# Performance work log

Hardware: AMD Instinct MI355X
Metric: run time of the kernel (lower is better)

The kernel has to match this reference:

```python
import jax, jax.numpy as jnp
import numpy as np

SOS = 1  # vocab.word2idx[SYM_SOS]


def _lstm_cell(x, h, c, Wih, Whh, b):
    # PyTorch LSTMCell gate order: i, f, g, o
    g = x @ Wih.T + h @ Whh.T + b
    i, f, gg, o = jnp.split(g, 4, axis=-1)
    c2 = jax.nn.sigmoid(f) * c + jax.nn.sigmoid(i) * jnp.tanh(gg)
    h2 = jax.nn.sigmoid(o) * jnp.tanh(c2)
    return h2, c2


def _attention(q, m, Wq, Wm, b, v):
    # additive attention: q [B,Dq], m [B,N,Dm] -> context [B,Dm]
    e = jnp.tanh((q @ Wq)[:, None, :] + m @ Wm + b)      # [B,N,H]
    score = jnp.einsum('bnh,h->bn', e, v)                # [B,N]
    a = jax.nn.softmax(score, axis=-1)
    return jnp.einsum('bn,bnd->bd', a, m)


def setup_inputs() -> dict:
    key = jax.random.key(0)
    ks = iter(jax.random.split(key, 32))
    B, T, V = 128, 20, 20000
    DI, DW, H = 512, 512, 1024
    s = 0.02
    d = {}
    d['img_feats'] = jax.random.normal(next(ks), (B, 36, DI), jnp.float32)
    d['ppl_feats'] = jax.random.normal(next(ks), (B, 100, DI), jnp.float32)
    d['answer_hint'] = jax.random.normal(next(ks), (B, DW), jnp.float32)
    d['question'] = jax.random.randint(next(ks), (B, T), 0, V)
    d['emb'] = jax.random.normal(next(ks), (V, DW), jnp.float32) * s
    d['pool_Wq'] = jax.random.normal(next(ks), (DW, DW), jnp.float32) * s
    d['pool_Wm'] = jax.random.normal(next(ks), (DI, DW), jnp.float32) * s
    d['pool_b'] = jnp.zeros((DW,), jnp.float32)
    d['pool_v'] = jax.random.normal(next(ks), (DW,), jnp.float32) * s
    d['img_Wq'] = jax.random.normal(next(ks), (H, H), jnp.float32) * s
    d['img_Wm'] = jax.random.normal(next(ks), (DI, H), jnp.float32) * s
    d['img_b'] = jnp.zeros((H,), jnp.float32)
    d['img_v'] = jax.random.normal(next(ks), (H,), jnp.float32) * s
    d['ppl_Wq'] = jax.random.normal(next(ks), (H, H), jnp.float32) * s
    d['ppl_Wm'] = jax.random.normal(next(ks), (DI, H), jnp.float32) * s
    d['ppl_b'] = jnp.zeros((H,), jnp.float32)
    d['ppl_v'] = jax.random.normal(next(ks), (H,), jnp.float32) * s
    d['vis_Wih'] = jax.random.normal(next(ks), (4 * H, DI + DW), jnp.float32) * s
    d['vis_Whh'] = jax.random.normal(next(ks), (4 * H, H), jnp.float32) * s
    d['vis_b'] = jnp.zeros((4 * H,), jnp.float32)
    d['lang_Wih'] = jax.random.normal(next(ks), (4 * H, H + DI), jnp.float32) * s
    d['lang_Whh'] = jax.random.normal(next(ks), (4 * H, H), jnp.float32) * s
    d['lang_b'] = jnp.zeros((4 * H,), jnp.float32)
    d['proj_W'] = jax.random.normal(next(ks), (H, V), jnp.float32) * s
    d['proj_b'] = jnp.zeros((V,), jnp.float32)
    return d


def reference(img_feats, ppl_feats, answer_hint, question, emb,
              pool_Wq, pool_Wm, pool_b, pool_v,
              img_Wq, img_Wm, img_b, img_v,
              ppl_Wq, ppl_Wm, ppl_b, ppl_v,
              vis_Wih, vis_Whh, vis_b,
              lang_Wih, lang_Whh, lang_b,
              proj_W, proj_b):
    B, T = question.shape
    H = vis_Whh.shape[1]
    # pooled image feature from answer hint (computed once)
    img_pool = _attention(answer_hint, img_feats, pool_Wq, pool_Wm, pool_b, pool_v)
    # teacher forcing inputs: SOS then question[:, :-1]
    tokens_in = jnp.concatenate(
        [jnp.full((B, 1), SOS, question.dtype), question[:, :-1]], axis=1)

    def step(carry, tok):
        h_vis, c_vis, h_lang, c_lang = carry
        dec_emb = jax.nn.relu(emb[tok])                          # [B,DW]
        x_vis = jnp.concatenate([img_pool, dec_emb], axis=-1)
        h_vis, c_vis = _lstm_cell(x_vis, h_vis, c_vis, vis_Wih, vis_Whh, vis_b)
        image_attn = _attention(h_vis, img_feats, img_Wq, img_Wm, img_b, img_v)
        ppl_attn = _attention(h_vis, ppl_feats, ppl_Wq, ppl_Wm, ppl_b, ppl_v)
        x_lang = jnp.concatenate([image_attn + ppl_attn, h_vis], axis=-1)
        h_lang, c_lang = _lstm_cell(x_lang, h_lang, c_lang, lang_Wih, lang_Whh, lang_b)
        logp = jax.nn.log_softmax(h_lang @ proj_W + proj_b, axis=-1)
        return (h_vis, c_vis, h_lang, c_lang), (logp, jnp.argmax(logp, axis=-1))

    z = jnp.zeros((B, H), img_feats.dtype)
    _, (logps, toks) = jax.lax.scan(step, (z, z, z, z), tokens_in.T)
    return jnp.transpose(logps, (1, 0, 2)), toks.T


if __name__ == '__main__':
    out = reference(**setup_inputs())
    print(out[0].shape, out[1].shape)
```

## Files before the change

### kernel.cpp

```cpp
#include <hip/hip_runtime.h>
#include <cstddef>
#include <cstdint>

using u16 = unsigned short;
typedef float    f32x4 __attribute__((ext_vector_type(4)));
typedef _Float16 f16x8 __attribute__((ext_vector_type(8)));
typedef u16      us8   __attribute__((ext_vector_type(8)));

constexpr int B  = 128;
constexpr int T  = 20;
constexpr int V  = 20000;
constexpr int DW = 512;
constexpr int H  = 1024;
constexpr int G4 = 4096;
constexpr int NI = 36;
constexpr int NP = 100;
constexpr int SOS = 1;

__device__ __forceinline__ float sigf(float x) { return 1.0f / (1.0f + expf(-x)); }
__device__ __forceinline__ u16 f16bits(_Float16 h) { u16 u; __builtin_memcpy(&u, &h, 2); return u; }
__device__ __forceinline__ float h2f(u16 u) { _Float16 h; __builtin_memcpy(&h, &u, 2); return (float)h; }

template<bool WSIDE>
__device__ __forceinline__ void split1(float x, u16& b0, u16& b1, u16& b2) {
    _Float16 h  = (_Float16)x;
    float    hf = (float)h;
    _Float16 lo = (_Float16)((x - hf) * 64.0f);
    _Float16 hs = (_Float16)(hf * (1.0f / 64.0f));
    b0 = f16bits(h);
    if constexpr (WSIDE) { b1 = f16bits(hs); b2 = f16bits(lo); }
    else                 { b1 = f16bits(lo); b2 = f16bits(hs); }
}

template<int BM, int BN, bool HAS_ADD, bool HAS_BIAS, int NSW = 0, bool OUTF16 = false>
__global__ __launch_bounds__(256)
void gemm3(const u16* __restrict__ A, const u16* __restrict__ Bt,
           const float* __restrict__ Add, const float* __restrict__ bias,
           void* __restrict__ Cv, int N, int K3)
{
    __shared__ __align__(16) u16 As[BM * 64];
    __shared__ __align__(16) u16 Bs[BN * 64];
    constexpr int FR = BM / 32, FC = BN / 32, PA = BM / 32, PB = BN / 32;
    const int tid  = threadIdx.x;
    int bx = blockIdx.x, by = blockIdx.y;
    if constexpr (NSW > 0) {
        const int nt = (int)gridDim.x, mt = (int)gridDim.y;
        const int lin = by * nt + bx;
        const int sc0 = (lin / (NSW * mt)) * NSW;
        const int w   = (NSW < nt - sc0) ? NSW : (nt - sc0);
        const int r   = lin - sc0 * mt;
        bx = sc0 + r % w;
        by = r / w;
    }
    const int bm   = by * BM, bn = bx * BN;
    const int lane = tid & 63, wid = tid >> 6;
    const int wm   = (wid >> 1) * (BM / 2), wn = (wid & 1) * (BN / 2);
    const int srow = tid >> 3;
    const int scol = (tid & 7) * 8;

    f32x4 acc[FR][FC] = {};
    us8 ra[PA], rb[PB];

    auto ldg = [&](int k0) {
#pragma unroll
        for (int p = 0; p < PA; ++p)
            ra[p] = *(const us8*)(A + (size_t)(bm + p * 32 + srow) * K3 + k0 + scol);
#pragma unroll
        for (int p = 0; p < PB; ++p) {
            int n = bn + p * 32 + srow; if (n > N - 1) n = N - 1;
            rb[p] = *(const us8*)(Bt + (size_t)n * K3 + k0 + scol);
        }
    };
    ldg(0);

    for (int k0 = 0; k0 < K3; k0 += 64) {
        __syncthreads();
#pragma unroll
        for (int p = 0; p < PA; ++p) {
            const int row = p * 32 + srow;
            *(us8*)((char*)As + row * 128 + ((scol * 2) ^ ((row & 7) << 4))) = ra[p];
        }
#pragma unroll
        for (int p = 0; p < PB; ++p) {
            const int row = p * 32 + srow;
            *(us8*)((char*)Bs + row * 128 + ((scol * 2) ^ ((row & 7) << 4))) = rb[p];
        }
        __syncthreads();
        if (k0 + 64 < K3) ldg(k0 + 64);
#pragma unroll
        for (int ks = 0; ks < 2; ++ks) {
            f16x8 af[FR], bf[FC];
#pragma unroll
            for (int m = 0; m < FR; ++m) {
                const int row = wm + m * 16 + (lane & 15);
                const int cb  = (ks * 64 + ((lane >> 4) << 4)) ^ ((row & 7) << 4);
                af[m] = *(const f16x8*)((const char*)As + row * 128 + cb);
            }
#pragma unroll
            for (int n = 0; n < FC; ++n) {
                const int row = wn + n * 16 + (lane & 15);
                const int cb  = (ks * 64 + ((lane >> 4) << 4)) ^ ((row & 7) << 4);
                bf[n] = *(const f16x8*)((const char*)Bs + row * 128 + cb);
            }
#pragma unroll
            for (int m = 0; m < FR; ++m)
#pragma unroll
                for (int n = 0; n < FC; ++n)
                    acc[m][n] = __builtin_amdgcn_mfma_f32_16x16x32_f16(af[m], bf[n], acc[m][n], 0, 0, 0);
        }
    }
#pragma unroll
    for (int m = 0; m < FR; ++m) {
        const int r0 = bm + wm + m * 16 + ((lane >> 4) << 2);
#pragma unroll
        for (int n = 0; n < FC; ++n) {
            const int c = bn + wn + n * 16 + (lane & 15);
            if (c < N) {
#pragma unroll
                for (int j = 0; j < 4; ++j) {
                    float v = acc[m][n][j];
                    if constexpr (HAS_ADD)  v += Add[(size_t)(r0 + j) * N + c];
                    if constexpr (HAS_BIAS) v += bias[c];
                    if constexpr (OUTF16)
                        ((u16*)Cv)[(size_t)(r0 + j) * N + c] = f16bits((_Float16)v);
                    else
                        ((float*)Cv)[(size_t)(r0 + j) * N + c] = v;
                }
            }
        }
    }
}

template<int EPI, int BN, int BK>
__device__ __forceinline__ void gemm_core(
    u16* __restrict__ As, u16* __restrict__ Bs,
    const u16* __restrict__ A, const u16* __restrict__ Bt,
    const float* __restrict__ Add, const float* __restrict__ bias,
    float* __restrict__ CS, u16* __restrict__ o1, u16* __restrict__ o2,
    int N, int K3, int t, int bx, int by)
{
    constexpr int NA8  = BK / 32;
    constexpr int TPRB = 256 / BN;
    constexpr int NB8  = (BK / TPRB) / 8;
    constexpr int NFC  = BN / 16;
    const int tid  = threadIdx.x;
    const int bn   = bx * BN, bm = by * 64;
    const int lane = tid & 63, wv = tid >> 6;
    const int rowA = tid >> 2;
    const int scA  = (tid & 3) * (BK / 4);
    const int rowB = tid / TPRB;
    const int scB  = (tid % TPRB) * (BK / TPRB);
    const int swzA = (rowA & 7) << 4;
    const int swzB = (rowB & 7) << 4;
    const u16* Ap = A  + (size_t)(bm + rowA) * K3 + scA;
    const u16* Bp = Bt + (size_t)(bn + rowB) * K3 + scB;
    char* Awp = (char*)As + rowA * (BK * 2);
    char* Bwp = (char*)Bs + rowB * (BK * 2);
    const int arow = wv * 16 + (lane & 15);
    const char* Arp = (const char*)As + arow * (BK * 2);
    const int aswz = (arow & 7) << 4;
    const int jl   = lane & 15;

    f32x4 acc[NFC] = {};
    us8 ra[NA8], rb[NB8];
#pragma unroll
    for (int i = 0; i < NA8; ++i) ra[i] = *(const us8*)(Ap + 8 * i);
#pragma unroll
    for (int i = 0; i < NB8; ++i) rb[i] = *(const us8*)(Bp + 8 * i);

    for (int k0 = 0; k0 < K3; k0 += BK) {
        __syncthreads();
#pragma unroll
        for (int i = 0; i < NA8; ++i)
            *(us8*)(Awp + ((scA * 2 + 16 * i) ^ swzA)) = ra[i];
#pragma unroll
        for (int i = 0; i < NB8; ++i)
            *(us8*)(Bwp + ((scB * 2 + 16 * i) ^ swzB)) = rb[i];
        __syncthreads();
        if (k0 + BK < K3) {
#pragma unroll
            for (int i = 0; i < NA8; ++i) ra[i] = *(const us8*)(Ap + k0 + BK + 8 * i);
#pragma unroll
            for (int i = 0; i < NB8; ++i) rb[i] = *(const us8*)(Bp + k0 + BK + 8 * i);
        }
#pragma unroll
        for (int ks = 0; ks < BK / 32; ++ks) {
            const int cb = ks * 64 + ((lane >> 4) << 4);
            const f16x8 af = *(const f16x8*)(Arp + (cb ^ aswz));
#pragma unroll
            for (int g = 0; g < NFC; ++g) {
                const int brow = g * 16 + jl;
                const f16x8 bf = *(const f16x8*)((const char*)Bs + brow * (BK * 2) + (cb ^ ((brow & 7) << 4)));
                acc[g] = __builtin_amdgcn_mfma_f32_16x16x32_f16(af, bf, acc[g], 0, 0, 0);
            }
        }
    }
    const int rb0 = bm + wv * 16 + ((lane >> 4) << 2);
    if constexpr (EPI == 0) {
#pragma unroll
        for (int g = 0; g < NFC; ++g) {
            const int c = bn + g * 16 + jl;
#pragma unroll
            for (int jj = 0; jj < 4; ++jj)
                CS[(size_t)(rb0 + jj) * N + c] = acc[g][jj];
        }
    } else {
        const int j = bx * 16 + jl;
#pragma unroll
        for (int jj = 0; jj < 4; ++jj) {
            const int b = rb0 + jj;
            float gi = acc[0][jj], gf = acc[1][jj], gg = acc[2][jj], go = acc[3][jj];
            if constexpr (EPI == 1) {
                const float* ap = Add + (size_t)b * 4096 + bn + jl;
                gi += ap[0]; gf += ap[16]; gg += ap[32]; go += ap[48];
            } else {
                const float* bp = bias + bn + jl;
                gi += bp[0]; gf += bp[16]; gg += bp[32]; go += bp[48];
            }
            const float c = sigf(gf) * CS[b * 1024 + j] + sigf(gi) * tanhf(gg);
            const float h = sigf(go) * tanhf(c);
            CS[b * 1024 + j] = c;
            u16 b0, b1, b2; split1<false>(h, b0, b1, b2);
            if constexpr (EPI == 1) {
                u16* a = o1 + (size_t)b * 3072 + j;
                a[0] = b0; a[1024] = b1; a[2048] = b2;
                u16* x = o2 + (size_t)b * 7680 + 512 + j;
                x[0] = b0; x[2560] = b1; x[5120] = b2;
            } else {
                u16* x = o1 + (size_t)b * 7680 + 1536 + j;
                x[0] = b0; x[2560] = b1; x[5120] = b2;
                u16* hh = o2 + ((size_t)b * T + t) * 3072 + j;
                hh[0] = b0; hh[1024] = b1; hh[2048] = b2;
            }
        }
    }
}

__global__ __launch_bounds__(256)
void gemm_q(const u16* __restrict__ A, const u16* __restrict__ Bt,
            float* __restrict__ CS, int N, int K3)
{
    __shared__ __align__(16) u16 As[64 * 384];
    __shared__ __align__(16) u16 Bs[32 * 384];
    gemm_core<0, 32, 384>(As, Bs, A, Bt, nullptr, nullptr, CS, nullptr, nullptr,
                          N, K3, 0, blockIdx.x, blockIdx.y);
}

__global__ __launch_bounds__(256)
void step_combo(const u16* __restrict__ lang_A, const u16* __restrict__ langW3,
                const float* __restrict__ lang_bi, float* __restrict__ c_lang,
                u16* __restrict__ lang_o1, u16* __restrict__ h3_all,
                const u16* __restrict__ vis_A, const u16* __restrict__ visWhh3,
                const float* __restrict__ g_pre_t, float* __restrict__ c_vis,
                u16* __restrict__ vis_o1, u16* __restrict__ vis_o2, int t)
{
    __shared__ __align__(16) u16 As[64 * 384];
    __shared__ __align__(16) u16 Bs[64 * 384];
    if (blockIdx.z == 0) {
        if (t >= 1)
            gemm_core<2, 64, 384>(As, Bs, lang_A, langW3, nullptr, lang_bi,
                                  c_lang, lang_o1, h3_all, G4, 7680, t - 1,
                                  blockIdx.x, blockIdx.y);
    } else {
        if (t < T)
            gemm_core<1, 64, 384>(As, Bs, vis_A, visWhh3, g_pre_t, nullptr,
                                  c_vis, vis_o1, vis_o2, G4, 3072, t,
                                  blockIdx.x, blockIdx.y);
    }
}

template<bool WSIDE>
__global__ __launch_bounds__(256)
void split3_rows(const float* __restrict__ src, int ld, int K8,
                 u16* __restrict__ out, int Kt, int coloff)
{
    const int idx = blockIdx.x * 256 + threadIdx.x;
    const int r = idx / K8, kk = (idx - r * K8) * 8;
    const float* s = src + (size_t)r * ld + kk;
    const float4 x0 = *(const float4*)s, x1 = *(const float4*)(s + 4);
    float xs[8] = {x0.x, x0.y, x0.z, x0.w, x1.x, x1.y, x1.z, x1.w};
    us8 h, m, l;
#pragma unroll
    for (int j = 0; j < 8; ++j) { u16 a, b, c; split1<WSIDE>(xs[j], a, b, c); h[j]=a; m[j]=b; l[j]=c; }
    u16* o = out + (size_t)r * (3 * Kt) + coloff + kk;
    *(us8*)o = h; *(us8*)(o + Kt) = m; *(us8*)(o + 2 * Kt) = l;
}

__global__ __launch_bounds__(256)
void split3_lstm(const float* __restrict__ src, int ld, int K8,
                 u16* __restrict__ out, int Kt, int coloff)
{
    const int idx = blockIdx.x * 256 + threadIdx.x;
    const int r = idx / K8, kk = (idx - r * K8) * 8;
    const int g = r >> 10, j = r & 1023;
    const int orow = ((j >> 4) << 6) + (g << 4) + (j & 15);
    const float* s = src + (size_t)r * ld + kk;
    const float4 x0 = *(const float4*)s, x1 = *(const float4*)(s + 4);
    float xs[8] = {x0.x, x0.y, x0.z, x0.w, x1.x, x1.y, x1.z, x1.w};
    us8 h, m, l;
#pragma unroll
    for (int jj = 0; jj < 8; ++jj) { u16 a, b, c; split1<true>(xs[jj], a, b, c); h[jj]=a; m[jj]=b; l[jj]=c; }
    u16* o = out + (size_t)orow * (3 * Kt) + coloff + kk;
    *(us8*)o = h; *(us8*)(o + Kt) = m; *(us8*)(o + 2 * Kt) = l;
}

__global__ __launch_bounds__(256)
void permute_bias_lstm(const float* __restrict__ b, float* __restrict__ out)
{
    const int c = blockIdx.x * 256 + threadIdx.x;
    const int jg = c >> 6, g = (c >> 4) & 3, jlo = c & 15;
    out[c] = b[g * 1024 + jg * 16 + jlo];
}

__global__ __launch_bounds__(256)
void transpose_split3_w(const float* __restrict__ W, int N, int K,
                        u16* __restrict__ out)
{
    const int n0 = blockIdx.x * 64, k0 = blockIdx.y * 64;
    const int tid = threadIdx.x;
    __shared__ float ts[64][65];
    for (int i = 0; i < 16; ++i) {
        const int idx = i * 256 + tid;
        const int kl = idx >> 6, nl = idx & 63;
        float v = 0.f;
        if (n0 + nl < N) v = W[(size_t)(k0 + kl) * N + n0 + nl];
        ts[nl][kl] = v;
    }
    __syncthreads();
    for (int i = 0; i < 2; ++i) {
        const int idx = i * 256 + tid;
        const int nl = idx >> 3, kc = (idx & 7) * 8;
        if (n0 + nl < N) {
            us8 h, m, l;
#pragma unroll
            for (int j = 0; j < 8; ++j) {
                u16 a, b, c; split1<true>(ts[nl][kc + j], a, b, c);
                h[j] = a; m[j] = b; l[j] = c;
            }
            u16* o = out + (size_t)(n0 + nl) * (3 * K) + k0 + kc;
            *(us8*)o = h; *(us8*)(o + K) = m; *(us8*)(o + 2 * K) = l;
        }
    }
}

__global__ __launch_bounds__(256)
void embed_relu3(const int* __restrict__ question, const float* __restrict__ emb,
                 u16* __restrict__ demb3)
{
    const int idx = blockIdx.x * 256 + threadIdx.x;
    const int r = idx >> 6, kk = (idx & 63) * 8;
    const int t = r / B, b = r - t * B;
    const int tok = (t == 0) ? SOS : question[b * T + t - 1];
    const float* s = emb + (size_t)tok * DW + kk;
    const float4 x0 = *(const float4*)s, x1 = *(const float4*)(s + 4);
    float xs[8] = {x0.x, x0.y, x0.z, x0.w, x1.x, x1.y, x1.z, x1.w};
    us8 h, m, l;
#pragma unroll
    for (int j = 0; j < 8; ++j) {
        u16 a, b2, c; split1<false>(fmaxf(xs[j], 0.f), a, b2, c);
        h[j] = a; m[j] = b2; l[j] = c;
    }
    u16* o = demb3 + (size_t)r * 1536 + kk;
    *(us8*)o = h; *(us8*)(o + 512) = m; *(us8*)(o + 1024) = l;
}

__global__ __launch_bounds__(256)
void attn_score(const float* __restrict__ q, int qld,
                const float* __restrict__ mW, const float* __restrict__ v,
                float* __restrict__ score, int Nn, int Hd)
{
    const int n = blockIdx.x, b = blockIdx.y;
    const float* qp = q + (size_t)b * qld;
    const float* mp = mW + ((size_t)b * Nn + n) * Hd;
    float s = 0.f;
    for (int h = threadIdx.x; h < Hd; h += 256)
        s += tanhf(qp[h] + mp[h]) * v[h];
    __shared__ float red[4];
    const int lane = threadIdx.x & 63, wv = threadIdx.x >> 6;
    for (int o = 32; o; o >>= 1) s += __shfl_down(s, o, 64);
    if (lane == 0) red[wv] = s;
    __syncthreads();
    if (threadIdx.x == 0) score[(size_t)b * Nn + n] = red[0] + red[1] + red[2] + red[3];
}

__global__ __launch_bounds__(256)
void attn_ctx_pool(const float* __restrict__ score, const float* __restrict__ m,
                   u16* __restrict__ out3, int Nn)
{
    constexpr int D = 512;
    const int b = blockIdx.x;
    __shared__ float aw[128];
    __shared__ float red[8];
    const int tid = threadIdx.x, lane = tid & 63, wv = tid >> 6;
    float mx = -3.4e38f;
    for (int n = tid; n < Nn; n += 256) mx = fmaxf(mx, score[(size_t)b * Nn + n]);
    for (int o = 32; o; o >>= 1) mx = fmaxf(mx, __shfl_down(mx, o, 64));
    if (lane == 0) red[wv] = mx;
    __syncthreads();
    mx = fmaxf(fmaxf(red[0], red[1]), fmaxf(red[2], red[3]));
    float se = 0.f;
    for (int n = tid; n < Nn; n += 256) {
        float e = expf(score[(size_t)b * Nn + n] - mx);
        aw[n] = e; se += e;
    }
    for (int o = 32; o; o >>= 1) se += __shfl_down(se, o, 64);
    if (lane == 0) red[4 + wv] = se;
    __syncthreads();
    const float inv = 1.0f / (red[4] + red[5] + red[6] + red[7]);
    for (int d = tid; d < D; d += 256) {
        float s = 0.f;
        for (int n = 0; n < Nn; ++n) s += aw[n] * m[((size_t)b * Nn + n) * D + d];
        s *= inv;
        u16 b0, b1, b2; split1<false>(s, b0, b1, b2);
        u16* o = out3 + (size_t)b * 1536 + d;
        o[0] = b0; o[512] = b1; o[1024] = b2;
    }
}

__global__ __launch_bounds__(512)
void attn_fused(const float* __restrict__ qbuf,
                const u16* __restrict__ img_mW, const u16* __restrict__ ppl_mW,
                const float* __restrict__ img_v, const float* __restrict__ ppl_v,
                const float* __restrict__ img_feats, const float* __restrict__ ppl_feats,
                u16* __restrict__ x3)
{
    const int b = blockIdx.x;
    const int tid = threadIdx.x, lane = tid & 63, wv = tid >> 6;
    __shared__ float qs[2048];
    __shared__ float vs[2048];
    __shared__ float aw[136];
    __shared__ float awn[136];

    for (int i = tid; i < 2048; i += 512) {
        qs[i] = qbuf[(size_t)b * 2048 + i];
        vs[i] = (i < 1024) ? img_v[i] : ppl_v[i - 1024];
    }
    __syncthreads();

    for (int n = wv; n < NI; n += 8) {
        const u16* mp = img_mW + ((size_t)b * NI + n) * 1024;
        float s = 0.f;
#pragma unroll
        for (int u = 0; u < 2; ++u) {
            const int h = (lane + 64 * u) * 8;
            const us8 m8 = *(const us8*)(mp + h);
#pragma unroll
            for (int j = 0; j < 8; ++j)
                s += tanhf(qs[h + j] + h2f(m8[j])) * vs[h + j];
        }
        for (int o = 1; o < 64; o <<= 1) s += __shfl_xor(s, o, 64);
        if (lane == 0) aw[n] = s;
    }
    for (int n = wv; n < NP; n += 8) {
        const u16* mp = ppl_mW + ((size_t)b * NP + n) * 1024;
        float s = 0.f;
#pragma unroll
        for (int u = 0; u < 2; ++u) {
            const int h = (lane + 64 * u) * 8;
            const us8 m8 = *(const us8*)(mp + h);
#pragma unroll
            for (int j = 0; j < 8; ++j)
                s += tanhf(qs[1024 + h + j] + h2f(m8[j])) * vs[1024 + h + j];
        }
        for (int o = 1; o < 64; o <<= 1) s += __shfl_xor(s, o, 64);
        if (lane == 0) aw[36 + n] = s;
    }
    __syncthreads();

    if (wv == 0) {
        const float x = (lane < NI) ? aw[lane] : -3.4e38f;
        float mx = x;
        for (int o = 1; o < 64; o <<= 1) mx = fmaxf(mx, __shfl_xor(mx, o, 64));
        const float e = (lane < NI) ? expf(x - mx) : 0.f;
        float ss = e;
        for (int o = 1; o < 64; o <<= 1) ss += __shfl_xor(ss, o, 64);
        if (lane < NI) awn[lane] = e / ss;
    } else if (wv == 1) {
        const float x0 = aw[36 + lane];
        const float x1 = (lane < NP - 64) ? aw[100 + lane] : -3.4e38f;
        float mx = fmaxf(x0, x1);
        for (int o = 1; o < 64; o <<= 1) mx = fmaxf(mx, __shfl_xor(mx, o, 64));
        const float e0 = expf(x0 - mx);
        const float e1 = (lane < NP - 64) ? expf(x1 - mx) : 0.f;
        float ss = e0 + e1;
        for (int o = 1; o < 64; o <<= 1) ss += __shfl_xor(ss, o, 64);
        awn[36 + lane] = e0 / ss;
        if (lane < NP - 64) awn[100 + lane] = e1 / ss;
    }
    __syncthreads();

    {
        const int d = tid;
        float s = 0.f;
        const float* ip = img_feats + (size_t)b * NI * 512 + d;
#pragma unroll 4
        for (int n = 0; n < NI; ++n) s += awn[n] * ip[n * 512];
        const float* pp = ppl_feats + (size_t)b * NP * 512 + d;
#pragma unroll 4
        for (int n = 0; n < NP; ++n) s += awn[36 + n] * pp[n * 512];
        u16 b0, b1, b2; split1<false>(s, b0, b1, b2);
        u16* o = x3 + (size_t)b * 7680 + d;
        o[0] = b0; o[2560] = b1; o[5120] = b2;
    }
}

__global__ __launch_bounds__(256)
void add_bcast(float* __restrict__ g_pre, const float* __restrict__ g_const)
{
    const int idx = blockIdx.x * 256 + threadIdx.x;
    const int bg = idx % (B * G4 / 4);
    float4 a = ((float4*)g_pre)[idx];
    const float4 c = ((const float4*)g_const)[bg];
    a.x += c.x; a.y += c.y; a.z += c.z; a.w += c.w;
    ((float4*)g_pre)[idx] = a;
}

__global__ __launch_bounds__(256)
void zero_f(float* __restrict__ p) { p[blockIdx.x * 256 + threadIdx.x] = 0.f; }

__global__ __launch_bounds__(256)
void zero_u32(unsigned int* __restrict__ p) { p[blockIdx.x * 256 + threadIdx.x] = 0u; }

__global__ __launch_bounds__(256)
void logsm_argmax(float* __restrict__ out)
{
    const int r = blockIdx.x;
    float* row = out + (size_t)r * V;
    const int tid = threadIdx.x, lane = tid & 63, wv = tid >> 6;
    float m = -3.4e38f, s = 0.f; int mi = 0;
    for (int i4 = tid; i4 < V / 4; i4 += 256) {
        const float4 x4 = ((const float4*)row)[i4];
        const float xs[4] = {x4.x, x4.y, x4.z, x4.w};
#pragma unroll
        for (int j = 0; j < 4; ++j) {
            const float x = xs[j];
            if (x > m) { s = s * expf(m - x) + 1.f; m = x; mi = i4 * 4 + j; }
            else       s += expf(x - m);
        }
    }
    for (int o = 1; o < 64; o <<= 1) {
        const float m2 = __shfl_xor(m, o, 64);
        const float s2 = __shfl_xor(s, o, 64);
        const int  mi2 = __shfl_xor(mi, o, 64);
        if (m2 > m || (m2 == m && mi2 < mi)) { s = s2 + s * expf(m - m2); m = m2; mi = mi2; }
        else s += s2 * expf(m2 - m);
    }
    __shared__ float sm[4], ssm[4]; __shared__ int smi[4];
    __shared__ float lse_sh; __shared__ int mi_sh;
    if (lane == 0) { sm[wv] = m; ssm[wv] = s; smi[wv] = mi; }
    __syncthreads();
    if (tid == 0) {
        float M = sm[0], S = ssm[0]; int MI = smi[0];
        for (int w = 1; w < 4; ++w) {
            if (sm[w] > M || (sm[w] == M && smi[w] < MI)) { S = ssm[w] + S * expf(M - sm[w]); M = sm[w]; MI = smi[w]; }
            else S += ssm[w] * expf(sm[w] - M);
        }
        lse_sh = M + logf(S); mi_sh = MI;
    }
    __syncthreads();
    const float lse = lse_sh;
    for (int i4 = tid; i4 < V / 4; i4 += 256) {
        float4 x4 = ((const float4*)row)[i4];
        x4.x -= lse; x4.y -= lse; x4.z -= lse; x4.w -= lse;
        ((float4*)row)[i4] = x4;
    }
    if (tid == 0) out[(size_t)B * T * V + r] = (float)mi_sh;
}

extern "C" void kernel_launch(void* const* d_in, const int* in_sizes, int n_in,
                              void* d_out, int out_size, void* d_ws, size_t ws_size,
                              hipStream_t stream)
{
    (void)in_sizes; (void)n_in; (void)out_size; (void)ws_size;

    const float* img_feats   = (const float*)d_in[0];
    const float* ppl_feats   = (const float*)d_in[1];
    const float* answer_hint = (const float*)d_in[2];
    const int*   question    = (const int*)d_in[3];
    const float* emb         = (const float*)d_in[4];
    const float* pool_Wq     = (const float*)d_in[5];
    const float* pool_Wm     = (const float*)d_in[6];
    const float* pool_b      = (const float*)d_in[7];
    const float* pool_v      = (const float*)d_in[8];
    const float* img_Wq      = (const float*)d_in[9];
    const float* img_Wm      = (const float*)d_in[10];
    const float* img_b       = (const float*)d_in[11];
    const float* img_v       = (const float*)d_in[12];
    const float* ppl_Wq      = (const float*)d_in[13];
    const float* ppl_Wm      = (const float*)d_in[14];
    const float* ppl_b       = (const float*)d_in[15];
    const float* ppl_v       = (const float*)d_in[16];
    const float* vis_Wih     = (const float*)d_in[17];
    const float* vis_Whh     = (const float*)d_in[18];
    const float* vis_b       = (const float*)d_in[19];
    const float* lang_Wih    = (const float*)d_in[20];
    const float* lang_Whh    = (const float*)d_in[21];
    const float* lang_b      = (const float*)d_in[22];
    const float* proj_W      = (const float*)d_in[23];
    const float* proj_b      = (const float*)d_in[24];

    float* out = (float*)d_out;
    float* ws  = (float*)d_ws;

    size_t off = 0;
    auto alloc = [&](size_t nf) { size_t r = off; off += (nf + 63) & ~(size_t)63; return r; };
    const size_t regionX = off;
    float* g_pre   = ws + alloc((size_t)T * B * G4);
    float* pool_mW = ws + alloc((size_t)B * NI * DW);
    u16*   demb3   = (u16*)(ws + alloc((size_t)T * B * 1536 / 2));
    u16*   hint3   = (u16*)(ws + alloc((size_t)B * 1536 / 2));
    u16*   poolWq3t= (u16*)(ws + alloc((size_t)512 * 1536 / 2));
    u16*   poolWm3t= (u16*)(ws + alloc((size_t)512 * 1536 / 2));
    u16*   visdemb3= (u16*)(ws + alloc((size_t)G4 * 1536 / 2));
    u16*   vispool3= (u16*)(ws + alloc((size_t)G4 * 1536 / 2));
    u16* img_mW    = (u16*)(ws + alloc((size_t)B * NI * H / 2));
    u16* ppl_mW    = (u16*)(ws + alloc((size_t)B * NP * H / 2));
    u16* img3      = (u16*)(ws + alloc((size_t)B * NI * 1536 / 2));
    u16* ppl3      = (u16*)(ws + alloc((size_t)B * NP * 1536 / 2));
    u16* imgpool3  = (u16*)(ws + alloc((size_t)B * 1536 / 2));
    u16* visWhh3   = (u16*)(ws + alloc((size_t)G4 * 3072 / 2));
    u16* langW3    = (u16*)(ws + alloc((size_t)G4 * 7680 / 2));
    u16* wq3t      = (u16*)(ws + alloc((size_t)2048 * 3072 / 2));
    u16* imgWm3t   = (u16*)(ws + alloc((size_t)1024 * 1536 / 2));
    u16* pplWm3t   = (u16*)(ws + alloc((size_t)1024 * 1536 / 2));
    float* c_vis   = ws + alloc((size_t)B * H);
    float* c_lang  = ws + alloc((size_t)B * H);
    u16* a3        = (u16*)(ws + alloc((size_t)2 * B * 3072 / 2));
    u16* x3        = (u16*)(ws + alloc((size_t)2 * B * 7680 / 2));
    u16* h3_all    = (u16*)(ws + alloc((size_t)B * T * 3072 / 2));
    float* qbuf    = ws + alloc((size_t)B * 2048);
    float* g_const = ws + alloc((size_t)B * G4);
    float* vis_bi  = ws + alloc((size_t)G4);
    float* lang_bi = ws + alloc((size_t)G4);
    float* pool_qW = ws + alloc((size_t)B * DW);
    float* pool_sc = ws + alloc((size_t)B * NI);
    u16* projW3t   = (u16*)(ws + regionX);

    const dim3 blk(256);

    zero_f<<<dim3((2 * B * H) / 256), blk, 0, stream>>>(c_vis);
    zero_u32<<<dim3((2 * B * 3072 + 2 * B * 7680) / 2 / 256), blk, 0, stream>>>((unsigned int*)a3);

    embed_relu3<<<dim3(T * B * 64 / 256), blk, 0, stream>>>(question, emb, demb3);
    permute_bias_lstm<<<dim3(16), blk, 0, stream>>>(vis_b, vis_bi);
    permute_bias_lstm<<<dim3(16), blk, 0, stream>>>(lang_b, lang_bi);
    split3_lstm<<<dim3(G4 * 64 / 256), blk, 0, stream>>>(vis_Wih + 512, 1024, 64, visdemb3, 512, 0);
    split3_lstm<<<dim3(G4 * 64 / 256), blk, 0, stream>>>(vis_Wih, 1024, 64, vispool3, 512, 0);
    split3_lstm<<<dim3(G4 * 128 / 256), blk, 0, stream>>>(vis_Whh, 1024, 128, visWhh3, 1024, 0);
    split3_lstm<<<dim3(G4 * 192 / 256), blk, 0, stream>>>(lang_Wih, 1536, 192, langW3, 2560, 0);
    split3_lstm<<<dim3(G4 * 128 / 256), blk, 0, stream>>>(lang_Whh, 1024, 128, langW3, 2560, 1536);
    split3_rows<false><<<dim3(B * NI * 64 / 256), blk, 0, stream>>>(img_feats, 512, 64, img3, 512, 0);
    split3_rows<false><<<dim3(B * NP * 64 / 256), blk, 0, stream>>>(ppl_feats, 512, 64, ppl3, 512, 0);
    split3_rows<false><<<dim3(B * 64 / 256), blk, 0, stream>>>(answer_hint, 512, 64, hint3, 512, 0);
    transpose_split3_w<<<dim3(8, 8), blk, 0, stream>>>(pool_Wq, 512, 512, poolWq3t);
    transpose_split3_w<<<dim3(8, 8), blk, 0, stream>>>(pool_Wm, 512, 512, poolWm3t);
    transpose_split3_w<<<dim3(16, 8), blk, 0, stream>>>(img_Wm, 1024, 512, imgWm3t);
    transpose_split3_w<<<dim3(16, 8), blk, 0, stream>>>(ppl_Wm, 1024, 512, pplWm3t);
    transpose_split3_w<<<dim3(16, 16), blk, 0, stream>>>(img_Wq, 1024, 1024, wq3t);
    transpose_split3_w<<<dim3(16, 16), blk, 0, stream>>>(ppl_Wq, 1024, 1024, wq3t + (size_t)1024 * 3072);

    gemm3<128, 128, false, true><<<dim3(32, 20), blk, 0, stream>>>(demb3, visdemb3, nullptr, vis_bi, g_pre, G4, 1536);
    gemm3<64, 64, false, false><<<dim3(8, 2), blk, 0, stream>>>(hint3, poolWq3t, nullptr, nullptr, pool_qW, 512, 1536);
    gemm3<128, 128, false, true><<<dim3(4, 36), blk, 0, stream>>>(img3, poolWm3t, nullptr, pool_b, pool_mW, 512, 1536);
    attn_score<<<dim3(NI, B), blk, 0, stream>>>(pool_qW, 512, pool_mW, pool_v, pool_sc, NI, 512);
    attn_ctx_pool<<<dim3(B), blk, 0, stream>>>(pool_sc, img_feats, imgpool3, NI);
    gemm3<64, 64, false, false><<<dim3(64, 2), blk, 0, stream>>>(imgpool3, vispool3, nullptr, nullptr, g_const, G4, 1536);
    add_bcast<<<dim3(T * B * G4 / 4 / 256), blk, 0, stream>>>(g_pre, g_const);
    gemm3<128, 128, false, true, 0, true><<<dim3(8, 36), blk, 0, stream>>>(img3, imgWm3t, nullptr, img_b, img_mW, H, 1536);
    gemm3<128, 128, false, true, 0, true><<<dim3(8, 100), blk, 0, stream>>>(ppl3, pplWm3t, nullptr, ppl_b, ppl_mW, H, 1536);

    for (int t = 0; t <= T; ++t) {
        u16* lang_A  = x3 + (size_t)((t + 1) & 1) * B * 7680;
        u16* lang_o1 = x3 + (size_t)(t & 1) * B * 7680;
        u16* vis_A   = a3 + (size_t)(t & 1) * B * 3072;
        u16* vis_o1  = a3 + (size_t)((t + 1) & 1) * B * 3072;
        u16* vis_o2  = x3 + (size_t)(t & 1) * B * 7680;
        const float* gp = g_pre + (size_t)(t < T ? t : 0) * B * G4;
        step_combo<<<dim3(64, 2, 2), blk, 0, stream>>>(
            lang_A, langW3, lang_bi, c_lang, lang_o1, h3_all,
            vis_A, visWhh3, gp, c_vis, vis_o1, vis_o2, t);
        if (t < T) {
            gemm_q<<<dim3(64, 2), blk, 0, stream>>>(vis_o1, wq3t, qbuf, 2048, 3072);
            attn_fused<<<dim3(B), dim3(512), 0, stream>>>(qbuf, img_mW, ppl_mW, img_v, ppl_v,
                                                          img_feats, ppl_feats, vis_o2);
        }
    }

    transpose_split3_w<<<dim3(313, 16), blk, 0, stream>>>(proj_W, V, 1024, projW3t);
    gemm3<128, 128, false, true, 20><<<dim3(157, 20), blk, 0, stream>>>(
        h3_all, projW3t, nullptr, proj_b, out, V, 3072);
    logsm_argmax<<<dim3(B * T), blk, 0, stream>>>(out);
}
```

Measured before the change: 3.658 ms.

## Reschedule recurrent step into two fused kernels overlapping attention, vis and lang LSTM

```diff
diff --git a/kernel.cpp b/kernel.cpp
--- a/kernel.cpp
+++ b/kernel.cpp
@@ -133,10 +133,10 @@
 
 template<int EPI, int BN, int BK>
 __device__ __forceinline__ void gemm_core(
-    u16* __restrict__ As, u16* __restrict__ Bs,
-    const u16* __restrict__ A, const u16* __restrict__ Bt,
-    const float* __restrict__ Add, const float* __restrict__ bias,
-    float* __restrict__ CS, u16* __restrict__ o1, u16* __restrict__ o2,
+    u16* As, u16* Bs,
+    const u16* A, const u16* Bt,
+    const float* Add, const float* bias,
+    float* CS, u16* o1, u16* o2,
     int N, int K3, int t, int bx, int by)
 {
     constexpr int NA8  = BK / 32;
@@ -236,208 +236,26 @@
     }
 }
 
-__global__ __launch_bounds__(256)
-void gemm_q(const u16* __restrict__ A, const u16* __restrict__ Bt,
-            float* __restrict__ CS, int N, int K3)
-{
-    __shared__ __align__(16) u16 As[64 * 384];
-    __shared__ __align__(16) u16 Bs[32 * 384];
-    gemm_core<0, 32, 384>(As, Bs, A, Bt, nullptr, nullptr, CS, nullptr, nullptr,
-                          N, K3, 0, blockIdx.x, blockIdx.y);
-}
-
-__global__ __launch_bounds__(256)
-void step_combo(const u16* __restrict__ lang_A, const u16* __restrict__ langW3,
-                const float* __restrict__ lang_bi, float* __restrict__ c_lang,
-                u16* __restrict__ lang_o1, u16* __restrict__ h3_all,
-                const u16* __restrict__ vis_A, const u16* __restrict__ visWhh3,
-                const float* __restrict__ g_pre_t, float* __restrict__ c_vis,
-                u16* __restrict__ vis_o1, u16* __restrict__ vis_o2, int t)
-{
-    __shared__ __align__(16) u16 As[64 * 384];
-    __shared__ __align__(16) u16 Bs[64 * 384];
-    if (blockIdx.z == 0) {
-        if (t >= 1)
-            gemm_core<2, 64, 384>(As, Bs, lang_A, langW3, nullptr, lang_bi,
-                                  c_lang, lang_o1, h3_all, G4, 7680, t - 1,
-                                  blockIdx.x, blockIdx.y);
-    } else {
-        if (t < T)
-            gemm_core<1, 64, 384>(As, Bs, vis_A, visWhh3, g_pre_t, nullptr,
-                                  c_vis, vis_o1, vis_o2, G4, 3072, t,
-                                  blockIdx.x, blockIdx.y);
-    }
-}
-
-template<bool WSIDE>
-__global__ __launch_bounds__(256)
-void split3_rows(const float* __restrict__ src, int ld, int K8,
-                 u16* __restrict__ out, int Kt, int coloff)
-{
-    const int idx = blockIdx.x * 256 + threadIdx.x;
-    const int r = idx / K8, kk = (idx - r * K8) * 8;
-    const float* s = src + (size_t)r * ld + kk;
-    const float4 x0 = *(const float4*)s, x1 = *(const float4*)(s + 4);
-    float xs[8] = {x0.x, x0.y, x0.z, x0.w, x1.x, x1.y, x1.z, x1.w};
-    us8 h, m, l;
-#pragma unroll
-    for (int j = 0; j < 8; ++j) { u16 a, b, c; split1<WSIDE>(xs[j], a, b, c); h[j]=a; m[j]=b; l[j]=c; }
-    u16* o = out + (size_t)r * (3 * Kt) + coloff + kk;
-    *(us8*)o = h; *(us8*)(o + Kt) = m; *(us8*)(o + 2 * Kt) = l;
-}
-
-__global__ __launch_bounds__(256)
-void split3_lstm(const float* __restrict__ src, int ld, int K8,
-                 u16* __restrict__ out, int Kt, int coloff)
-{
-    const int idx = blockIdx.x * 256 + threadIdx.x;
-    const int r = idx / K8, kk = (idx - r * K8) * 8;
-    const int g = r >> 10, j = r & 1023;
-    const int orow = ((j >> 4) << 6) + (g << 4) + (j & 15);
-    const float* s = src + (size_t)r * ld + kk;
-    const float4 x0 = *(const float4*)s, x1 = *(const float4*)(s + 4);
-    float xs[8] = {x0.x, x0.y, x0.z, x0.w, x1.x, x1.y, x1.z, x1.w};
-    us8 h, m, l;
-#pragma unroll
-    for (int jj = 0; jj < 8; ++jj) { u16 a, b, c; split1<true>(xs[jj], a, b, c); h[jj]=a; m[jj]=b; l[jj]=c; }
-    u16* o = out + (size_t)orow * (3 * Kt) + coloff + kk;
-    *(us8*)o = h; *(us8*)(o + Kt) = m; *(us8*)(o + 2 * Kt) = l;
-}
-
-__global__ __launch_bounds__(256)
-void permute_bias_lstm(const float* __restrict__ b, float* __restrict__ out)
-{
-    const int c = blockIdx.x * 256 + threadIdx.x;
-    const int jg = c >> 6, g = (c >> 4) & 3, jlo = c & 15;
-    out[c] = b[g * 1024 + jg * 16 + jlo];
-}
-
-__global__ __launch_bounds__(256)
-void transpose_split3_w(const float* __restrict__ W, int N, int K,
-                        u16* __restrict__ out)
-{
-    const int n0 = blockIdx.x * 64, k0 = blockIdx.y * 64;
-    const int tid = threadIdx.x;
-    __shared__ float ts[64][65];
-    for (int i = 0; i < 16; ++i) {
-        const int idx = i * 256 + tid;
-        const int kl = idx >> 6, nl = idx & 63;
-        float v = 0.f;
-        if (n0 + nl < N) v = W[(size_t)(k0 + kl) * N + n0 + nl];
-        ts[nl][kl] = v;
-    }
-    __syncthreads();
-    for (int i = 0; i < 2; ++i) {
-        const int idx = i * 256 + tid;
-        const int nl = idx >> 3, kc = (idx & 7) * 8;
-        if (n0 + nl < N) {
-            us8 h, m, l;
-#pragma unroll
-            for (int j = 0; j < 8; ++j) {
-                u16 a, b, c; split1<true>(ts[nl][kc + j], a, b, c);
-                h[j] = a; m[j] = b; l[j] = c;
-            }
-            u16* o = out + (size_t)(n0 + nl) * (3 * K) + k0 + kc;
-            *(us8*)o = h; *(us8*)(o + K) = m; *(us8*)(o + 2 * K) = l;
-        }
-    }
-}
-
-__global__ __launch_bounds__(256)
-void embed_relu3(const int* __restrict__ question, const float* __restrict__ emb,
-                 u16* __restrict__ demb3)
-{
-    const int idx = blockIdx.x * 256 + threadIdx.x;
-    const int r = idx >> 6, kk = (idx & 63) * 8;
-    const int t = r / B, b = r - t * B;
-    const int tok = (t == 0) ? SOS : question[b * T + t - 1];
-    const float* s = emb + (size_t)tok * DW + kk;
-    const float4 x0 = *(const float4*)s, x1 = *(const float4*)(s + 4);
-    float xs[8] = {x0.x, x0.y, x0.z, x0.w, x1.x, x1.y, x1.z, x1.w};
-    us8 h, m, l;
-#pragma unroll
-    for (int j = 0; j < 8; ++j) {
-        u16 a, b2, c; split1<false>(fmaxf(xs[j], 0.f), a, b2, c);
-        h[j] = a; m[j] = b2; l[j] = c;
-    }
-    u16* o = demb3 + (size_t)r * 1536 + kk;
-    *(us8*)o = h; *(us8*)(o + 512) = m; *(us8*)(o + 1024) = l;
-}
-
-__global__ __launch_bounds__(256)
-void attn_score(const float* __restrict__ q, int qld,
-                const float* __restrict__ mW, const float* __restrict__ v,
-                float* __restrict__ score, int Nn, int Hd)
-{
-    const int n = blockIdx.x, b = blockIdx.y;
-    const float* qp = q + (size_t)b * qld;
-    const float* mp = mW + ((size_t)b * Nn + n) * Hd;
-    float s = 0.f;
-    for (int h = threadIdx.x; h < Hd; h += 256)
-        s += tanhf(qp[h] + mp[h]) * v[h];
-    __shared__ float red[4];
-    const int lane = threadIdx.x & 63, wv = threadIdx.x >> 6;
-    for (int o = 32; o; o >>= 1) s += __shfl_down(s, o, 64);
-    if (lane == 0) red[wv] = s;
-    __syncthreads();
-    if (threadIdx.x == 0) score[(size_t)b * Nn + n] = red[0] + red[1] + red[2] + red[3];
-}
-
-__global__ __launch_bounds__(256)
-void attn_ctx_pool(const float* __restrict__ score, const float* __restrict__ m,
-                   u16* __restrict__ out3, int Nn)
-{
-    constexpr int D = 512;
-    const int b = blockIdx.x;
-    __shared__ float aw[128];
-    __shared__ float red[8];
+__device__ __forceinline__ void attn_body(
+    int b, const float* __restrict__ qbuf,
+    const u16* __restrict__ img_mW, const u16* __restrict__ ppl_mW,
+    const float* __restrict__ img_v, const float* __restrict__ ppl_v,
+    const float* __restrict__ img_feats, const float* __restrict__ ppl_feats,
+    u16* __restrict__ x3_out, float* smf)
+{
     const int tid = threadIdx.x, lane = tid & 63, wv = tid >> 6;
-    float mx = -3.4e38f;
-    for (int n = tid; n < Nn; n += 256) mx = fmaxf(mx, score[(size_t)b * Nn + n]);
-    for (int o = 32; o; o >>= 1) mx = fmaxf(mx, __shfl_down(mx, o, 64));
-    if (lane == 0) red[wv] = mx;
-    __syncthreads();
-    mx = fmaxf(fmaxf(red[0], red[1]), fmaxf(red[2], red[3]));
-    float se = 0.f;
-    for (int n = tid; n < Nn; n += 256) {
-        float e = expf(score[(size_t)b * Nn + n] - mx);
-        aw[n] = e; se += e;
-    }
-    for (int o = 32; o; o >>= 1) se += __shfl_down(se, o, 64);
-    if (lane == 0) red[4 + wv] = se;
-    __syncthreads();
-    const float inv = 1.0f / (red[4] + red[5] + red[6] + red[7]);
-    for (int d = tid; d < D; d += 256) {
-        float s = 0.f;
-        for (int n = 0; n < Nn; ++n) s += aw[n] * m[((size_t)b * Nn + n) * D + d];
-        s *= inv;
-        u16 b0, b1, b2; split1<false>(s, b0, b1, b2);
-        u16* o = out3 + (size_t)b * 1536 + d;
-        o[0] = b0; o[512] = b1; o[1024] = b2;
-    }
-}
-
-__global__ __launch_bounds__(512)
-void attn_fused(const float* __restrict__ qbuf,
-                const u16* __restrict__ img_mW, const u16* __restrict__ ppl_mW,
-                const float* __restrict__ img_v, const float* __restrict__ ppl_v,
-                const float* __restrict__ img_feats, const float* __restrict__ ppl_feats,
-                u16* __restrict__ x3)
-{
-    const int b = blockIdx.x;
-    const int tid = threadIdx.x, lane = tid & 63, wv = tid >> 6;
-    __shared__ float qs[2048];
-    __shared__ float vs[2048];
-    __shared__ float aw[136];
-    __shared__ float awn[136];
-
-    for (int i = tid; i < 2048; i += 512) {
+    float* qs  = smf;
+    float* vs  = smf + 2048;
+    float* aw  = smf + 4096;
+    float* awn = smf + 4352;
+
+    for (int i = tid; i < 2048; i += 256) {
         qs[i] = qbuf[(size_t)b * 2048 + i];
         vs[i] = (i < 1024) ? img_v[i] : ppl_v[i - 1024];
     }
     __syncthreads();
 
-    for (int n = wv; n < NI; n += 8) {
+    for (int n = wv; n < NI; n += 4) {
         const u16* mp = img_mW + ((size_t)b * NI + n) * 1024;
         float s = 0.f;
 #pragma unroll
@@ -451,7 +269,7 @@
         for (int o = 1; o < 64; o <<= 1) s += __shfl_xor(s, o, 64);
         if (lane == 0) aw[n] = s;
     }
-    for (int n = wv; n < NP; n += 8) {
+    for (int n = wv; n < NP; n += 4) {
         const u16* mp = ppl_mW + ((size_t)b * NP + n) * 1024;
         float s = 0.f;
 #pragma unroll
@@ -489,8 +307,9 @@
     }
     __syncthreads();
 
-    {
-        const int d = tid;
+#pragma unroll
+    for (int dd = 0; dd < 2; ++dd) {
+        const int d = tid + dd * 256;
         float s = 0.f;
         const float* ip = img_feats + (size_t)b * NI * 512 + d;
 #pragma unroll 4
@@ -499,20 +318,205 @@
 #pragma unroll 4
         for (int n = 0; n < NP; ++n) s += awn[36 + n] * pp[n * 512];
         u16 b0, b1, b2; split1<false>(s, b0, b1, b2);
-        u16* o = x3 + (size_t)b * 7680 + d;
+        u16* o = x3_out + (size_t)b * 7680 + d;
         o[0] = b0; o[2560] = b1; o[5120] = b2;
     }
 }
 
 __global__ __launch_bounds__(256)
-void add_bcast(float* __restrict__ g_pre, const float* __restrict__ g_const)
+void step_k1(const float* __restrict__ qbuf,
+             const u16* __restrict__ img_mW, const u16* __restrict__ ppl_mW,
+             const float* __restrict__ img_v, const float* __restrict__ ppl_v,
+             const float* __restrict__ img_feats, const float* __restrict__ ppl_feats,
+             u16* x3_prev,
+             const u16* __restrict__ vis_A, const u16* __restrict__ visWhh3,
+             const float* __restrict__ g_pre_t, float* c_vis,
+             u16* a3_new, u16* x3_cur, int t)
+{
+    __shared__ __align__(16) u16 smem[2 * 64 * 192];
+    const int blk = blockIdx.x;
+    if (blk < 128) {
+        if (t >= 1)
+            attn_body(blk, qbuf, img_mW, ppl_mW, img_v, ppl_v,
+                      img_feats, ppl_feats, x3_prev, (float*)smem);
+    } else {
+        if (t < T)
+            gemm_core<1, 64, 192>(smem, smem + 64 * 192, vis_A, visWhh3,
+                                  g_pre_t, nullptr, c_vis, a3_new, x3_cur,
+                                  G4, 3072, t, (blk - 128) & 63, (blk - 128) >> 6);
+    }
+}
+
+__global__ __launch_bounds__(256)
+void step_k2(const u16* __restrict__ a3_new, const u16* __restrict__ wq3t,
+             float* qbuf,
+             const u16* __restrict__ lang_A, const u16* __restrict__ langW3,
+             const float* __restrict__ lang_bi, float* c_lang,
+             u16* lang_o1, u16* h3_all, int t)
+{
+    __shared__ __align__(16) u16 smem[2 * 64 * 192];
+    const int blk = blockIdx.x;
+    if (blk < 128) {
+        if (t < T)
+            gemm_core<0, 32, 192>(smem, smem + 64 * 192, a3_new, wq3t,
+                                  nullptr, nullptr, qbuf, nullptr, nullptr,
+                                  2048, 3072, t, blk & 63, blk >> 6);
+    } else {
+        if (t >= 1)
+            gemm_core<2, 64, 192>(smem, smem + 64 * 192, lang_A, langW3,
+                                  nullptr, lang_bi, c_lang, lang_o1, h3_all,
+                                  G4, 7680, t - 1, (blk - 128) & 63, (blk - 128) >> 6);
+    }
+}
+
+template<bool WSIDE>
+__global__ __launch_bounds__(256)
+void split3_rows(const float* __restrict__ src, int ld, int K8,
+                 u16* __restrict__ out, int Kt, int coloff)
 {
     const int idx = blockIdx.x * 256 + threadIdx.x;
-    const int bg = idx % (B * G4 / 4);
-    float4 a = ((float4*)g_pre)[idx];
-    const float4 c = ((const float4*)g_const)[bg];
-    a.x += c.x; a.y += c.y; a.z += c.z; a.w += c.w;
-    ((float4*)g_pre)[idx] = a;
+    const int r = idx / K8, kk = (idx - r * K8) * 8;
+    const float* s = src + (size_t)r * ld + kk;
+    const float4 x0 = *(const float4*)s, x1 = *(const float4*)(s + 4);
+    float xs[8] = {x0.x, x0.y, x0.z, x0.w, x1.x, x1.y, x1.z, x1.w};
+    us8 h, m, l;
+#pragma unroll
+    for (int j = 0; j < 8; ++j) { u16 a, b, c; split1<WSIDE>(xs[j], a, b, c); h[j]=a; m[j]=b; l[j]=c; }
+    u16* o = out + (size_t)r * (3 * Kt) + coloff + kk;
+    *(us8*)o = h; *(us8*)(o + Kt) = m; *(us8*)(o + 2 * Kt) = l;
+}
+
+__global__ __launch_bounds__(256)
+void split3_lstm(const float* __restrict__ src, int ld, int K8,
+                 u16* __restrict__ out, int Kt, int coloff)
+{
+    const int idx = blockIdx.x * 256 + threadIdx.x;
+    const int r = idx / K8, kk = (idx - r * K8) * 8;
+    const int g = r >> 10, j = r & 1023;
+    const int orow = ((j >> 4) << 6) + (g << 4) + (j & 15);
+    const float* s = src + (size_t)r * ld + kk;
+    const float4 x0 = *(const float4*)s, x1 = *(const float4*)(s + 4);
+    float xs[8] = {x0.x, x0.y, x0.z, x0.w, x1.x, x1.y, x1.z, x1.w};
+    us8 h, m, l;
+#pragma unroll
+    for (int jj = 0; jj < 8; ++jj) { u16 a, b, c; split1<true>(xs[jj], a, b, c); h[jj]=a; m[jj]=b; l[jj]=c; }
+    u16* o = out + (size_t)orow * (3 * Kt) + coloff + kk;
+    *(us8*)o = h; *(us8*)(o + Kt) = m; *(us8*)(o + 2 * Kt) = l;
+}
+
+__global__ __launch_bounds__(256)
+void permute_bias_lstm(const float* __restrict__ b, float* __restrict__ out)
+{
+    const int c = blockIdx.x * 256 + threadIdx.x;
+    const int jg = c >> 6, g = (c >> 4) & 3, jlo = c & 15;
+    out[c] = b[g * 1024 + jg * 16 + jlo];
+}
+
+__global__ __launch_bounds__(256)
+void transpose_split3_w(const float* __restrict__ W, int N, int K,
+                        u16* __restrict__ out)
+{
+    const int n0 = blockIdx.x * 64, k0 = blockIdx.y * 64;
+    const int tid = threadIdx.x;
+    __shared__ float ts[64][65];
+    for (int i = 0; i < 16; ++i) {
+        const int idx = i * 256 + tid;
+        const int kl = idx >> 6, nl = idx & 63;
+        float v = 0.f;
+        if (n0 + nl < N) v = W[(size_t)(k0 + kl) * N + n0 + nl];
+        ts[nl][kl] = v;
+    }
+    __syncthreads();
+    for (int i = 0; i < 2; ++i) {
+        const int idx = i * 256 + tid;
+        const int nl = idx >> 3, kc = (idx & 7) * 8;
+        if (n0 + nl < N) {
+            us8 h, m, l;
+#pragma unroll
+            for (int j = 0; j < 8; ++j) {
+                u16 a, b, c; split1<true>(ts[nl][kc + j], a, b, c);
+                h[j] = a; m[j] = b; l[j] = c;
+            }
+            u16* o = out + (size_t)(n0 + nl) * (3 * K) + k0 + kc;
+            *(us8*)o = h; *(us8*)(o + K) = m; *(us8*)(o + 2 * K) = l;
+        }
+    }
+}
+
+__global__ __launch_bounds__(256)
+void embed_relu3(const int* __restrict__ question, const float* __restrict__ emb,
+                 u16* __restrict__ A2)
+{
+    const int idx = blockIdx.x * 256 + threadIdx.x;
+    const int r = idx >> 6, kk = (idx & 63) * 8;
+    const int t = r / B, b = r - t * B;
+    const int tok = (t == 0) ? SOS : question[b * T + t - 1];
+    const float* s = emb + (size_t)tok * DW + kk;
+    const float4 x0 = *(const float4*)s, x1 = *(const float4*)(s + 4);
+    float xs[8] = {x0.x, x0.y, x0.z, x0.w, x1.x, x1.y, x1.z, x1.w};
+    us8 h, m, l;
+#pragma unroll
+    for (int j = 0; j < 8; ++j) {
+        u16 a, b2, c; split1<false>(fmaxf(xs[j], 0.f), a, b2, c);
+        h[j] = a; m[j] = b2; l[j] = c;
+    }
+    u16* o = A2 + (size_t)r * 3072 + 512 + kk;
+    *(us8*)o = h; *(us8*)(o + 1024) = m; *(us8*)(o + 2048) = l;
+}
+
+__global__ __launch_bounds__(256)
+void attn_score(const float* __restrict__ q, int qld,
+                const float* __restrict__ mW, const float* __restrict__ v,
+                float* __restrict__ score, int Nn, int Hd)
+{
+    const int n = blockIdx.x, b = blockIdx.y;
+    const float* qp = q + (size_t)b * qld;
+    const float* mp = mW + ((size_t)b * Nn + n) * Hd;
+    float s = 0.f;
+    for (int h = threadIdx.x; h < Hd; h += 256)
+        s += tanhf(qp[h] + mp[h]) * v[h];
+    __shared__ float red[4];
+    const int lane = threadIdx.x & 63, wv = threadIdx.x >> 6;
+    for (int o = 32; o; o >>= 1) s += __shfl_down(s, o, 64);
+    if (lane == 0) red[wv] = s;
+    __syncthreads();
+    if (threadIdx.x == 0) score[(size_t)b * Nn + n] = red[0] + red[1] + red[2] + red[3];
+}
+
+__global__ __launch_bounds__(256)
+void attn_ctx_pool(const float* __restrict__ score, const float* __restrict__ m,
+                   u16* __restrict__ A2, int Nn)
+{
+    constexpr int D = 512;
+    const int b = blockIdx.x;
+    __shared__ float aw[128];
+    __shared__ float red[8];
+    const int tid = threadIdx.x, lane = tid & 63, wv = tid >> 6;
+    float mx = -3.4e38f;
+    for (int n = tid; n < Nn; n += 256) mx = fmaxf(mx, score[(size_t)b * Nn + n]);
+    for (int o = 32; o; o >>= 1) mx = fmaxf(mx, __shfl_down(mx, o, 64));
+    if (lane == 0) red[wv] = mx;
+    __syncthreads();
+    mx = fmaxf(fmaxf(red[0], red[1]), fmaxf(red[2], red[3]));
+    float se = 0.f;
+    for (int n = tid; n < Nn; n += 256) {
+        float e = expf(score[(size_t)b * Nn + n] - mx);
+        aw[n] = e; se += e;
+    }
+    for (int o = 32; o; o >>= 1) se += __shfl_down(se, o, 64);
+    if (lane == 0) red[4 + wv] = se;
+    __syncthreads();
+    const float inv = 1.0f / (red[4] + red[5] + red[6] + red[7]);
+    for (int d = tid; d < D; d += 256) {
+        float s = 0.f;
+        for (int n = 0; n < Nn; ++n) s += aw[n] * m[((size_t)b * Nn + n) * D + d];
+        s *= inv;
+        u16 b0, b1, b2; split1<false>(s, b0, b1, b2);
+        for (int tt = 0; tt < T; ++tt) {
+            u16* o = A2 + ((size_t)tt * B + b) * 3072 + d;
+            o[0] = b0; o[1024] = b1; o[2048] = b2;
+        }
+    }
 }
 
 __global__ __launch_bounds__(256)
@@ -607,17 +611,15 @@
     const size_t regionX = off;
     float* g_pre   = ws + alloc((size_t)T * B * G4);
     float* pool_mW = ws + alloc((size_t)B * NI * DW);
-    u16*   demb3   = (u16*)(ws + alloc((size_t)T * B * 1536 / 2));
+    u16*   A2      = (u16*)(ws + alloc((size_t)T * B * 3072 / 2));
     u16*   hint3   = (u16*)(ws + alloc((size_t)B * 1536 / 2));
     u16*   poolWq3t= (u16*)(ws + alloc((size_t)512 * 1536 / 2));
     u16*   poolWm3t= (u16*)(ws + alloc((size_t)512 * 1536 / 2));
-    u16*   visdemb3= (u16*)(ws + alloc((size_t)G4 * 1536 / 2));
-    u16*   vispool3= (u16*)(ws + alloc((size_t)G4 * 1536 / 2));
-    u16* img_mW    = (u16*)(ws + alloc((size_t)B * NI * H / 2));
-    u16* ppl_mW    = (u16*)(ws + alloc((size_t)B * NP * H / 2));
-    u16* img3      = (u16*)(ws + alloc((size_t)B * NI * 1536 / 2));
-    u16* ppl3      = (u16*)(ws + alloc((size_t)B * NP * 1536 / 2));
-    u16* imgpool3  = (u16*)(ws + alloc((size_t)B * 1536 / 2));
+    u16*   visWih3 = (u16*)(ws + alloc((size_t)G4 * 3072 / 2));
+    u16*   img_mW  = (u16*)(ws + alloc((size_t)B * NI * H / 2));
+    u16*   ppl_mW  = (u16*)(ws + alloc((size_t)B * NP * H / 2));
+    u16*   img3    = (u16*)(ws + alloc((size_t)B * NI * 1536 / 2));
+    u16*   ppl3    = (u16*)(ws + alloc((size_t)B * NP * 1536 / 2));
     u16* visWhh3   = (u16*)(ws + alloc((size_t)G4 * 3072 / 2));
     u16* langW3    = (u16*)(ws + alloc((size_t)G4 * 7680 / 2));
     u16* wq3t      = (u16*)(ws + alloc((size_t)2048 * 3072 / 2));
@@ -629,7 +631,6 @@
     u16* x3        = (u16*)(ws + alloc((size_t)2 * B * 7680 / 2));
     u16* h3_all    = (u16*)(ws + alloc((size_t)B * T * 3072 / 2));
     float* qbuf    = ws + alloc((size_t)B * 2048);
-    float* g_const = ws + alloc((size_t)B * G4);
     float* vis_bi  = ws + alloc((size_t)G4);
     float* lang_bi = ws + alloc((size_t)G4);
     float* pool_qW = ws + alloc((size_t)B * DW);
@@ -641,11 +642,10 @@
     zero_f<<<dim3((2 * B * H) / 256), blk, 0, stream>>>(c_vis);
     zero_u32<<<dim3((2 * B * 3072 + 2 * B * 7680) / 2 / 256), blk, 0, stream>>>((unsigned int*)a3);
 
-    embed_relu3<<<dim3(T * B * 64 / 256), blk, 0, stream>>>(question, emb, demb3);
+    embed_relu3<<<dim3(T * B * 64 / 256), blk, 0, stream>>>(question, emb, A2);
     permute_bias_lstm<<<dim3(16), blk, 0, stream>>>(vis_b, vis_bi);
     permute_bias_lstm<<<dim3(16), blk, 0, stream>>>(lang_b, lang_bi);
-    split3_lstm<<<dim3(G4 * 64 / 256), blk, 0, stream>>>(vis_Wih + 512, 1024, 64, visdemb3, 512, 0);
-    split3_lstm<<<dim3(G4 * 64 / 256), blk, 0, stream>>>(vis_Wih, 1024, 64, vispool3, 512, 0);
+    split3_lstm<<<dim3(G4 * 128 / 256), blk, 0, stream>>>(vis_Wih, 1024, 128, visWih3, 1024, 0);
     split3_lstm<<<dim3(G4 * 128 / 256), blk, 0, stream>>>(vis_Whh, 1024, 128, visWhh3, 1024, 0);
     split3_lstm<<<dim3(G4 * 192 / 256), blk, 0, stream>>>(lang_Wih, 1536, 192, langW3, 2560, 0);
     split3_lstm<<<dim3(G4 * 128 / 256), blk, 0, stream>>>(lang_Whh, 1024, 128, langW3, 2560, 1536);
@@ -659,31 +659,26 @@
     transpose_split3_w<<<dim3(16, 16), blk, 0, stream>>>(img_Wq, 1024, 1024, wq3t);
     transpose_split3_w<<<dim3(16, 16), blk, 0, stream>>>(ppl_Wq, 1024, 1024, wq3t + (size_t)1024 * 3072);
 
-    gemm3<128, 128, false, true><<<dim3(32, 20), blk, 0, stream>>>(demb3, visdemb3, nullptr, vis_bi, g_pre, G4, 1536);
     gemm3<64, 64, false, false><<<dim3(8, 2), blk, 0, stream>>>(hint3, poolWq3t, nullptr, nullptr, pool_qW, 512, 1536);
     gemm3<128, 128, false, true><<<dim3(4, 36), blk, 0, stream>>>(img3, poolWm3t, nullptr, pool_b, pool_mW, 512, 1536);
     attn_score<<<dim3(NI, B), blk, 0, stream>>>(pool_qW, 512, pool_mW, pool_v, pool_sc, NI, 512);
-    attn_ctx_pool<<<dim3(B), blk, 0, stream>>>(pool_sc, img_feats, imgpool3, NI);
-    gemm3<64, 64, false, false><<<dim3(64, 2), blk, 0, stream>>>(imgpool3, vispool3, nullptr, nullptr, g_const, G4, 1536);
-    add_bcast<<<dim3(T * B * G4 / 4 / 256), blk, 0, stream>>>(g_pre, g_const);
+    attn_ctx_pool<<<dim3(B), blk, 0, stream>>>(pool_sc, img_feats, A2, NI);
+    gemm3<128, 128, false, true><<<dim3(32, 20), blk, 0, stream>>>(A2, visWih3, nullptr, vis_bi, g_pre, G4, 3072);
     gemm3<128, 128, false, true, 0, true><<<dim3(8, 36), blk, 0, stream>>>(img3, imgWm3t, nullptr, img_b, img_mW, H, 1536);
     gemm3<128, 128, false, true, 0, true><<<dim3(8, 100), blk, 0, stream>>>(ppl3, pplWm3t, nullptr, ppl_b, ppl_mW, H, 1536);
 
     for (int t = 0; t <= T; ++t) {
-        u16* lang_A  = x3 + (size_t)((t + 1) & 1) * B * 7680;
-        u16* lang_o1 = x3 + (size_t)(t & 1) * B * 7680;
-        u16* vis_A   = a3 + (size_t)(t & 1) * B * 3072;
-        u16* vis_o1  = a3 + (size_t)((t + 1) & 1) * B * 3072;
-        u16* vis_o2  = x3 + (size_t)(t & 1) * B * 7680;
+        u16* x3_prev = x3 + (size_t)((t + 1) & 1) * B * 7680;
+        u16* x3_cur  = x3 + (size_t)(t & 1) * B * 7680;
+        u16* vis_Ain = a3 + (size_t)(t & 1) * B * 3072;
+        u16* a3_new  = a3 + (size_t)((t + 1) & 1) * B * 3072;
         const float* gp = g_pre + (size_t)(t < T ? t : 0) * B * G4;
-        step_combo<<<dim3(64, 2, 2), blk, 0, stream>>>(
-            lang_A, langW3, lang_bi, c_lang, lang_o1, h3_all,
-            vis_A, visWhh3, gp, c_vis, vis_o1, vis_o2, t);
-        if (t < T) {
-            gemm_q<<<dim3(64, 2), blk, 0, stream>>>(vis_o1, wq3t, qbuf, 2048, 3072);
-            attn_fused<<<dim3(B), dim3(512), 0, stream>>>(qbuf, img_mW, ppl_mW, img_v, ppl_v,
-                                                          img_feats, ppl_feats, vis_o2);
-        }
+        step_k1<<<dim3(256), blk, 0, stream>>>(
+            qbuf, img_mW, ppl_mW, img_v, ppl_v, img_feats, ppl_feats, x3_prev,
+            vis_Ain, visWhh3, gp, c_vis, a3_new, x3_cur, t);
+        step_k2<<<dim3(256), blk, 0, stream>>>(
+            a3_new, wq3t, qbuf, x3_prev, langW3, lang_bi, c_lang,
+            x3_cur, h3_all, t);
     }
 
     transpose_split3_w<<<dim3(313, 16), blk, 0, stream>>>(proj_W, V, 1024, projW3t);
```

Measured after the change: 4.016 ms. 9.8% more time.
